# Kernel tuning notes

Measured on AMD Instinct MI355X. Metric: run time of the kernel, lower is better.

## Reference

```python
import jax, jax.numpy as jnp
import numpy as np

V, D, H, S, L, B = 32000, 1024, 4096, 2048, 2, 4
EPS = 1e-5

def setup_inputs() -> dict:
    key = jax.random.key(0)
    ks = jax.random.split(key, 20)
    n = lambda k, shp, s=0.02: (jax.random.normal(k, shp, dtype=jnp.float32) * s)
    inp = {
        'x': jax.random.randint(ks[0], (B, S), 0, V),
        'emb': n(ks[1], (V, D)),
        'wq': n(ks[2], (L, D, H)), 'bq': jnp.zeros((L, H), jnp.float32),
        'wk': n(ks[3], (L, D, H)), 'bk': jnp.zeros((L, H), jnp.float32),
        'wv': n(ks[4], (L, D, H)), 'bv': jnp.zeros((L, H), jnp.float32),
        'wo': n(ks[5], (L, H, D)), 'bo': jnp.zeros((L, D), jnp.float32),
        'w1': n(ks[6], (L, D, H)), 'b1': jnp.zeros((L, H), jnp.float32),
        'w2': n(ks[7], (L, H, D)), 'b2': jnp.zeros((L, D), jnp.float32),
        'ln1_w': jnp.ones((L, S, D), jnp.float32), 'ln1_b': jnp.zeros((L, S, D), jnp.float32),
        'ln2_w': jnp.ones((L, S, D), jnp.float32), 'ln2_b': jnp.zeros((L, S, D), jnp.float32),
    }
    return inp

def _pos_encoding(seq_len, dim, dtype):
    pos = jnp.arange(seq_len, dtype=dtype)          # [S]
    i = jnp.arange(dim, dtype=dtype)                # [D]
    div = jnp.power(jnp.asarray(10000.0, dtype), i / dim)
    ang = pos[:, None] / div[None, :]               # [S, D]
    return jnp.where((jnp.arange(dim) % 2) == 0, jnp.sin(ang), jnp.cos(ang))

def _layernorm2d(y, w, b):
    # normalize over last two dims (token_size, n_dim), per sample
    m = jnp.mean(y, axis=(-2, -1), keepdims=True)
    v = jnp.var(y, axis=(-2, -1), keepdims=True)
    return (y - m) * jax.lax.rsqrt(v + EPS) * w + b

def reference(x, emb, wq, bq, wk, bk, wv, bv, wo, bo, w1, b1, w2, b2, ln1_w, ln1_b, ln2_w, ln2_b):
    y = emb[x]                                       # [B, S, D]
    y = y + _pos_encoding(y.shape[1], y.shape[2], y.dtype)
    n_blocks = wq.shape[0]
    for l in range(n_blocks):
        q = jnp.einsum('bsd,dh->bsh', y, wq[l]) + bq[l]
        k = jnp.einsum('bsd,dh->bsh', y, wk[l]) + bk[l]
        v = jnp.einsum('bsd,dh->bsh', y, wv[l]) + bv[l]
        scores = jnp.einsum('bqh,bkh->bqk', q, k)    # NOTE: unscaled, as in source
        att = jnp.einsum('bqk,bkh->bqh', jax.nn.softmax(scores, axis=-1), v)
        att = jnp.einsum('bsh,hd->bsd', att, wo[l]) + bo[l]
        y = _layernorm2d(y + att, ln1_w[l], ln1_b[l])
        h = jnp.einsum('bsd,dh->bsh', y, w1[l]) + b1[l]
        ffn = jax.nn.gelu(jnp.einsum('bsh,hd->bsd', h, w2[l]) + b2[l], approximate=False)  # GELU AFTER linear2, as in source
        y = _layernorm2d(y + ffn, ln2_w[l], ln2_b[l])
    return y
```

## Files before the change

kernel.cpp:

```cpp
#include <hip/hip_runtime.h>
#include <cstdint>
#include <cstddef>

using bf16 = __bf16;
using f16  = _Float16;
typedef float f32x4 __attribute__((ext_vector_type(4)));
typedef bf16 bf16x8 __attribute__((ext_vector_type(8)));
typedef bf16 bf16x4 __attribute__((ext_vector_type(4)));
typedef f16  f16x8  __attribute__((ext_vector_type(8)));
typedef f16  f16x4  __attribute__((ext_vector_type(4)));

#define NB 4
#define SEQ 2048
#define DM 1024
#define HD 4096
#define SD (SEQ*DM)

__device__ __forceinline__ float geluf(float v) {
    return 0.5f * v * (1.0f + erff(v * 0.70710678118654752f));
}

#define GLL(gp, lp) __builtin_amdgcn_global_load_lds( \
    (const __attribute__((address_space(1))) void*)(gp), \
    (__attribute__((address_space(3))) void*)(lp), 16, 0, 0)

template<int EPI, bool BIAS, int NP, int DT>
__global__ __launch_bounds__(256, NP == 1 ? 4 : 2) void gemm3_nt(
    const bf16* __restrict__ Ah, const bf16* __restrict__ Al,
    const bf16* __restrict__ Bh, const bf16* __restrict__ Bl,
    const float* __restrict__ bias, void* __restrict__ Cg, void* __restrict__ Cl,
    const int K, const int ldab, const int ldc,
    const long sA, const long sB, const long sC)
{
    constexpr int TILE = 128 * 64;
    constexpr int LOSZ = (NP == 3) ? TILE : 8;
    __shared__ __align__(16) bf16 smAh[TILE];
    __shared__ __align__(16) bf16 smBh[TILE];
    __shared__ __align__(16) bf16 smAl[LOSZ];
    __shared__ __align__(16) bf16 smBl[LOSZ];

    const int tid  = threadIdx.x;
    const int lane = tid & 63;
    const int wave = tid >> 6;
    const int wr   = (wave >> 1) << 6;
    const int wc   = (wave & 1) << 6;
    const int l15  = lane & 15;
    const int q4   = lane >> 4;

    int bx = blockIdx.x, by = blockIdx.y;
    {
        const int gx = gridDim.x, gy = gridDim.y;
        if (((gx & 3) | (gy & 3)) == 0) {
            const int tot = gx * gy;
            const int n   = bx + gx * by;
            const int l   = (n & 7) * (tot >> 3) + (n >> 3);
            const int st  = l >> 4, pos = l & 15;
            bx = (st % (gx >> 2)) * 4 + (pos & 3);
            by = (st / (gx >> 2)) * 4 + (pos >> 2);
        }
    }

    const long aoff = (long)blockIdx.z * sA + (long)bx * 128 * ldab;
    const long boff = (long)blockIdx.z * sB + (long)by * 128 * ldab;
    const bf16* pAh = Ah + aoff;
    const bf16* pAl = (NP == 3) ? Al + aoff : nullptr;
    const bf16* pBh = Bh + boff;
    const bf16* pBl = (NP == 3) ? Bl + boff : nullptr;

    int srow[4], scol[4];
#pragma unroll
    for (int it = 0; it < 4; ++it) {
        int chunk = it * 256 + tid;
        int m = chunk >> 3;
        srow[it] = m;
        scol[it] = ((chunk & 7) ^ (m & 7)) * 8;
    }

    f32x4 acc[4][4] = {};

    for (int k0 = 0; k0 < K; k0 += 64) {
#pragma unroll
        for (int it = 0; it < 4; ++it) {
            const long go = (long)srow[it] * ldab + (k0 + scol[it]);
            const size_t lo = (size_t)(it * 256 + (wave << 6)) * 8;
            GLL(pAh + go, smAh + lo);
            if constexpr (NP == 3) GLL(pAl + go, smAl + lo);
            GLL(pBh + go, smBh + lo);
            if constexpr (NP == 3) GLL(pBl + go, smBl + lo);
        }
        __syncthreads();

#pragma unroll
        for (int kk = 0; kk < 2; ++kk) {
            bf16x8 avh[4], avl[4], bvh[4], bvl[4];
#pragma unroll
            for (int i = 0; i < 4; ++i) {
                const int rowa = wr + i * 16 + l15;
                const int ca = ((kk * 4 + q4) ^ (rowa & 7)) * 8;
                avh[i] = *(const bf16x8*)(smAh + rowa * 64 + ca);
                if constexpr (NP == 3) avl[i] = *(const bf16x8*)(smAl + rowa * 64 + ca);
                const int rowb = wc + i * 16 + l15;
                const int cb = ((kk * 4 + q4) ^ (rowb & 7)) * 8;
                bvh[i] = *(const bf16x8*)(smBh + rowb * 64 + cb);
                if constexpr (NP == 3) bvl[i] = *(const bf16x8*)(smBl + rowb * 64 + cb);
            }
#pragma unroll
            for (int i = 0; i < 4; ++i)
#pragma unroll
                for (int j = 0; j < 4; ++j) {
                    if constexpr (DT == 1) {
                        acc[i][j] = __builtin_amdgcn_mfma_f32_16x16x32_f16(
                            *(const f16x8*)&avh[i], *(const f16x8*)&bvh[j],
                            acc[i][j], 0, 0, 0);
                    } else {
                        acc[i][j] = __builtin_amdgcn_mfma_f32_16x16x32_bf16(
                            avh[i], bvh[j], acc[i][j], 0, 0, 0);
                        if constexpr (NP == 3) {
                            acc[i][j] = __builtin_amdgcn_mfma_f32_16x16x32_bf16(
                                avl[i], bvh[j], acc[i][j], 0, 0, 0);
                            acc[i][j] = __builtin_amdgcn_mfma_f32_16x16x32_bf16(
                                avh[i], bvl[j], acc[i][j], 0, 0, 0);
                        }
                    }
                }
        }
        __syncthreads();
    }

    const long zC = (long)blockIdx.z * sC;
    const int gcol0 = by * 128 + wc + l15;
    const int grow0 = bx * 128 + wr + q4 * 4;
#pragma unroll
    for (int j = 0; j < 4; ++j) {
        const int col = gcol0 + j * 16;
        const float bvz = BIAS ? bias[col] : 0.0f;
#pragma unroll
        for (int i = 0; i < 4; ++i) {
            const int row = grow0 + i * 16;
            if (EPI == 5) {
                bf16x4 oh, ol;
#pragma unroll
                for (int e = 0; e < 4; ++e) {
                    const float v = acc[i][j][e] + bvz;
                    const bf16 hi = (bf16)v;
                    oh[e] = hi;
                    ol[e] = (bf16)(v - (float)hi);
                }
                *(bf16x4*)((bf16*)Cg + zC + (long)col * ldc + row) = oh;
                *(bf16x4*)((bf16*)Cl + zC + (long)col * ldc + row) = ol;
            } else if (EPI == 7) {
                f16x4 o;
#pragma unroll
                for (int e = 0; e < 4; ++e) o[e] = (f16)(acc[i][j][e] + bvz);
                *(f16x4*)((f16*)Cg + zC + (long)col * ldc + row) = o;
            } else {
#pragma unroll
                for (int e = 0; e < 4; ++e) {
                    float v = acc[i][j][e] + bvz;
                    if (EPI == 1) v = geluf(v);
                    const long off = zC + (long)(row + e) * ldc + col;
                    if (EPI == 4) {
                        const bf16 hi = (bf16)v;
                        ((bf16*)Cg)[off] = hi;
                        ((bf16*)Cl)[off] = (bf16)(v - (float)hi);
                    } else if (EPI == 6) {
                        ((f16*)Cg)[off] = (f16)v;
                    } else {
                        ((float*)Cg)[off] = v;
                    }
                }
            }
        }
    }
}

__global__ __launch_bounds__(256) void embed_k(
    const int* __restrict__ x, const float* __restrict__ emb,
    bf16* __restrict__ yh, bf16* __restrict__ yl, f16* __restrict__ yf16,
    const float* __restrict__ wkbq, float* __restrict__ vb)
{
    const int bs = blockIdx.x;
    const int s = bs & (SEQ - 1);
    const long e0 = (long)x[bs] * DM;
    const int d = threadIdx.x * 4;
    const float4 ev = *(const float4*)(emb + e0 + d);
    float o[4];
    const float fs = (float)s;
#pragma unroll
    for (int e = 0; e < 4; ++e) {
        const int dd = d + e;
        const float div = powf(10000.0f, (float)dd * (1.0f / 1024.0f));
        const float ang = fs / div;
        const float p = (dd & 1) ? cosf(ang) : sinf(ang);
        o[e] = ((const float*)&ev)[e] + p;
    }
    bf16x4 oh, ol; f16x4 of;
#pragma unroll
    for (int e = 0; e < 4; ++e) {
        oh[e] = (bf16)o[e];
        ol[e] = (bf16)(o[e] - (float)oh[e]);
        of[e] = (f16)o[e];
    }
    *(bf16x4*)(yh + (long)bs * DM + d) = oh;
    *(bf16x4*)(yl + (long)bs * DM + d) = ol;
    *(f16x4*) (yf16 + (long)bs * DM + d) = of;
    const float4 wv = *(const float4*)(wkbq + d);
    float sdot = o[0] * wv.x + o[1] * wv.y + o[2] * wv.z + o[3] * wv.w;
#pragma unroll
    for (int off = 32; off; off >>= 1) sdot += __shfl_xor(sdot, off);
    __shared__ float red[4];
    if ((threadIdx.x & 63) == 0) red[threadIdx.x >> 6] = sdot;
    __syncthreads();
    if (threadIdx.x == 0) vb[bs] = red[0] + red[1] + red[2] + red[3];
}

__global__ __launch_bounds__(256) void copy_split_k(
    const float* __restrict__ src, bf16* __restrict__ dh, bf16* __restrict__ dl)
{
    const long i = ((long)blockIdx.x * 256 + threadIdx.x) * 4;
    const float4 v = *(const float4*)(src + i);
    const float vv[4] = {v.x, v.y, v.z, v.w};
    bf16x4 oh, ol;
#pragma unroll
    for (int e = 0; e < 4; ++e) {
        const bf16 hi = (bf16)vv[e];
        oh[e] = hi;
        ol[e] = (bf16)(vv[e] - (float)hi);
    }
    *(bf16x4*)(dh + i) = oh;
    *(bf16x4*)(dl + i) = ol;
}

__global__ __launch_bounds__(256) void reduce8s_k(
    const float* __restrict__ p, bf16* __restrict__ dh, bf16* __restrict__ dl,
    f16* __restrict__ df)
{
    const long i = ((long)blockIdx.x * 256 + threadIdx.x) * 4;
    const long PL = (long)1 << 20;
    float vv[4] = {0.f, 0.f, 0.f, 0.f};
#pragma unroll
    for (int q = 0; q < 8; ++q) {
        const float4 a = *(const float4*)(p + q * PL + i);
        vv[0] += a.x; vv[1] += a.y; vv[2] += a.z; vv[3] += a.w;
    }
    bf16x4 oh, ol; f16x4 of;
#pragma unroll
    for (int e = 0; e < 4; ++e) {
        const bf16 hi = (bf16)vv[e];
        oh[e] = hi;
        ol[e] = (bf16)(vv[e] - (float)hi);
        of[e] = (f16)vv[e];
    }
    *(bf16x4*)(dh + i) = oh;
    *(bf16x4*)(dl + i) = ol;
    *(f16x4*) (df + i) = of;
}

__global__ __launch_bounds__(256) void reduce8t_k(
    const float* __restrict__ p, bf16* __restrict__ dsth, bf16* __restrict__ dstl,
    f16* __restrict__ dstf)
{
    __shared__ float tf[64][65];
    const long PL = (long)1 << 20;
    const int c0 = blockIdx.x * 64, r0 = blockIdx.y * 64;
    const int t = threadIdx.x;
    const int tr = t >> 4;
    const int tc = (t & 15) * 4;
#pragma unroll
    for (int pp = 0; pp < 4; ++pp) {
        const int r = tr + pp * 16;
        float vv[4] = {0.f, 0.f, 0.f, 0.f};
#pragma unroll
        for (int q = 0; q < 8; ++q) {
            const float4 v = *(const float4*)(p + q * PL + (long)(r0 + r) * 1024 + c0 + tc);
            vv[0] += v.x; vv[1] += v.y; vv[2] += v.z; vv[3] += v.w;
        }
#pragma unroll
        for (int e = 0; e < 4; ++e) tf[r][tc + e] = vv[e];
    }
    __syncthreads();
#pragma unroll
    for (int pp = 0; pp < 4; ++pp) {
        const int c = tr + pp * 16;
        bf16x4 oh, ol; f16x4 of;
#pragma unroll
        for (int e = 0; e < 4; ++e) {
            const float v = tf[tc + e][c];
            const bf16 hi = (bf16)v;
            oh[e] = hi;
            ol[e] = (bf16)(v - (float)hi);
            of[e] = (f16)v;
        }
        *(bf16x4*)(dsth + (long)(c0 + c) * 1024 + r0 + tc) = oh;
        *(bf16x4*)(dstl + (long)(c0 + c) * 1024 + r0 + tc) = ol;
        *(f16x4*) (dstf + (long)(c0 + c) * 1024 + r0 + tc) = of;
    }
}

__global__ __launch_bounds__(256) void transpose_k(
    const float* __restrict__ src, bf16* __restrict__ dsth, bf16* __restrict__ dstl,
    int R, int C)
{
    __shared__ bf16 th[64][65];
    __shared__ bf16 tl[64][65];
    const int c0 = blockIdx.x * 64, r0 = blockIdx.y * 64;
    const int t = threadIdx.x;
    const int tr = t >> 4;
    const int tc = (t & 15) * 4;
#pragma unroll
    for (int p = 0; p < 4; ++p) {
        const int r = tr + p * 16;
        const float4 v = *(const float4*)(src + (long)(r0 + r) * C + c0 + tc);
        const float vv[4] = {v.x, v.y, v.z, v.w};
#pragma unroll
        for (int e = 0; e < 4; ++e) {
            const bf16 hi = (bf16)vv[e];
            th[r][tc + e] = hi;
            tl[r][tc + e] = (bf16)(vv[e] - (float)hi);
        }
    }
    __syncthreads();
#pragma unroll
    for (int p = 0; p < 4; ++p) {
        const int c = tr + p * 16;
        bf16x4 oh, ol;
#pragma unroll
        for (int e = 0; e < 4; ++e) { oh[e] = th[tc + e][c]; ol[e] = tl[tc + e][c]; }
        *(bf16x4*)(dsth + (long)(c0 + c) * R + r0 + tc) = oh;
        *(bf16x4*)(dstl + (long)(c0 + c) * R + r0 + tc) = ol;
    }
}

__global__ __launch_bounds__(256) void matvec_wb_k(
    const float* __restrict__ W, const float* __restrict__ b, float* __restrict__ out)
{
    const int d = blockIdx.x;
    const int t = threadIdx.x;
    float s = 0.f;
    for (int h = t * 4; h < HD; h += 1024) {
        const float4 wv = *(const float4*)(W + (long)d * HD + h);
        const float4 bv = *(const float4*)(b + h);
        s += wv.x * bv.x + wv.y * bv.y + wv.z * bv.z + wv.w * bv.w;
    }
#pragma unroll
    for (int o = 32; o; o >>= 1) s += __shfl_xor(s, o);
    __shared__ float red[4];
    if ((t & 63) == 0) red[t >> 6] = s;
    __syncthreads();
    if (t == 0) out[d] = red[0] + red[1] + red[2] + red[3];
}

__global__ __launch_bounds__(256) void matvec_bt_k(
    const bf16* __restrict__ bth, const bf16* __restrict__ btl,
    const float* __restrict__ b, const float* __restrict__ add,
    float* __restrict__ out)
{
    const int j = blockIdx.x;
    const int t = threadIdx.x;
    float s = 0.f;
    for (int h = t * 4; h < HD; h += 1024) {
        const bf16x4 hx = *(const bf16x4*)(bth + (long)j * HD + h);
        const bf16x4 lx = *(const bf16x4*)(btl + (long)j * HD + h);
        const float4 bv = *(const float4*)(b + h);
        s += ((float)hx[0] + (float)lx[0]) * bv.x + ((float)hx[1] + (float)lx[1]) * bv.y
           + ((float)hx[2] + (float)lx[2]) * bv.z + ((float)hx[3] + (float)lx[3]) * bv.w;
    }
#pragma unroll
    for (int o = 32; o; o >>= 1) s += __shfl_xor(s, o);
    __shared__ float red[4];
    if ((t & 63) == 0) red[t >> 6] = s;
    __syncthreads();
    if (t == 0) out[j] = red[0] + red[1] + red[2] + red[3] + add[j];
}

__global__ __launch_bounds__(256) void softmax_k(
    const float* __restrict__ S, const float* __restrict__ v,
    f16* __restrict__ P)
{
    const long row = blockIdx.x;
    const float4* src = (const float4*)(S + (row << 11));
    const float* vr = v + (long)(row >> 11) * SEQ;
    const int t = threadIdx.x;
    float4 a = src[t], b = src[256 + t];
    const float4 va = *(const float4*)(vr + t * 4);
    const float4 vb = *(const float4*)(vr + 1024 + t * 4);
    a.x += va.x; a.y += va.y; a.z += va.z; a.w += va.w;
    b.x += vb.x; b.y += vb.y; b.z += vb.z; b.w += vb.w;
    float m = fmaxf(fmaxf(fmaxf(a.x, a.y), fmaxf(a.z, a.w)),
                    fmaxf(fmaxf(b.x, b.y), fmaxf(b.z, b.w)));
#pragma unroll
    for (int o = 32; o; o >>= 1) m = fmaxf(m, __shfl_xor(m, o));
    __shared__ float red1[4], red2[4];
    const int wv = t >> 6;
    if ((t & 63) == 0) red1[wv] = m;
    __syncthreads();
    m = fmaxf(fmaxf(red1[0], red1[1]), fmaxf(red1[2], red1[3]));

    a.x = expf(a.x - m); a.y = expf(a.y - m); a.z = expf(a.z - m); a.w = expf(a.w - m);
    b.x = expf(b.x - m); b.y = expf(b.y - m); b.z = expf(b.z - m); b.w = expf(b.w - m);
    float s = a.x + a.y + a.z + a.w + b.x + b.y + b.z + b.w;
#pragma unroll
    for (int o = 32; o; o >>= 1) s += __shfl_xor(s, o);
    if ((t & 63) == 0) red2[wv] = s;
    __syncthreads();
    s = red2[0] + red2[1] + red2[2] + red2[3];
    const float inv = 1.0f / s;

    f16x4 o0, o1;
    o0[0] = (f16)(a.x * inv); o0[1] = (f16)(a.y * inv);
    o0[2] = (f16)(a.z * inv); o0[3] = (f16)(a.w * inv);
    o1[0] = (f16)(b.x * inv); o1[1] = (f16)(b.y * inv);
    o1[2] = (f16)(b.z * inv); o1[3] = (f16)(b.w * inv);
    *(f16x4*)(P + (row << 11) + t * 4) = o0;
    *(f16x4*)(P + (row << 11) + 1024 + t * 4) = o1;
}

__global__ __launch_bounds__(256) void ln_stats_k(
    const bf16* __restrict__ yh, const bf16* __restrict__ yl,
    const float* __restrict__ r, float2* __restrict__ part)
{
    const int b = blockIdx.y;
    const long base = (long)b * SD + (long)blockIdx.x * (SD / 64);
    float s = 0.f, q = 0.f;
    for (int i = threadIdx.x; i < (SD / 64) / 4; i += 256) {
        const bf16x4 h = *(const bf16x4*)(yh + base + i * 4);
        const bf16x4 l = *(const bf16x4*)(yl + base + i * 4);
        const float4 c = *(const float4*)(r + base + i * 4);
        const float cc[4] = {c.x, c.y, c.z, c.w};
#pragma unroll
        for (int e = 0; e < 4; ++e) {
            const float xx = (float)h[e] + (float)l[e] + cc[e];
            s += xx; q += xx * xx;
        }
    }
#pragma unroll
    for (int o = 32; o; o >>= 1) { s += __shfl_xor(s, o); q += __shfl_xor(q, o); }
    __shared__ float rs[4], rq[4];
    const int wv = threadIdx.x >> 6;
    if ((threadIdx.x & 63) == 0) { rs[wv] = s; rq[wv] = q; }
    __syncthreads();
    if (threadIdx.x == 0)
        part[b * 64 + blockIdx.x] = make_float2(rs[0] + rs[1] + rs[2] + rs[3],
                                                rq[0] + rq[1] + rq[2] + rq[3]);
}

__global__ void ln_fin_k(const float2* __restrict__ part, float2* __restrict__ stats)
{
    const int b = blockIdx.x;
    const float2 p = part[b * 64 + threadIdx.x];
    float s = p.x, q = p.y;
#pragma unroll
    for (int o = 32; o; o >>= 1) { s += __shfl_xor(s, o); q += __shfl_xor(q, o); }
    if (threadIdx.x == 0) {
        const float inv_n = 1.0f / (float)SD;
        const float mean = s * inv_n;
        const float var = fmaxf(q * inv_n - mean * mean, 0.f);
        stats[b] = make_float2(mean, rsqrtf(var + 1e-5f));
    }
}

__global__ __launch_bounds__(256) void ln_apply_k(
    const bf16* __restrict__ yh_in, const bf16* __restrict__ yl_in,
    const float* __restrict__ r,
    const float* __restrict__ w, const float* __restrict__ bb,
    const float2* __restrict__ stats,
    bf16* __restrict__ yh_out, bf16* __restrict__ yl_out, f16* __restrict__ yf16,
    float* __restrict__ fout,
    const float* __restrict__ wkbq, float* __restrict__ vb)
{
    const long i = (long)blockIdx.x * 1024 + threadIdx.x * 4;
    const int smp = (int)(i >> 21);
    const long sd = i & (SD - 1);
    const float2 st = stats[smp];
    const bf16x4 h = *(const bf16x4*)(yh_in + i);
    const bf16x4 l = *(const bf16x4*)(yl_in + i);
    const float4 c = *(const float4*)(r + i);
    const float4 wv = *(const float4*)(w + sd);
    const float4 bv = *(const float4*)(bb + sd);
    const float cc[4] = {c.x, c.y, c.z, c.w};
    const float ww[4] = {wv.x, wv.y, wv.z, wv.w};
    const float bbx[4] = {bv.x, bv.y, bv.z, bv.w};
    float o[4];
#pragma unroll
    for (int e = 0; e < 4; ++e) {
        const float xx = (float)h[e] + (float)l[e] + cc[e];
        o[e] = (xx - st.x) * st.y * ww[e] + bbx[e];
    }
    bf16x4 oh, ol; f16x4 of;
#pragma unroll
    for (int e = 0; e < 4; ++e) {
        oh[e] = (bf16)o[e];
        ol[e] = (bf16)(o[e] - (float)oh[e]);
        of[e] = (f16)o[e];
    }
    *(bf16x4*)(yh_out + i) = oh;
    *(bf16x4*)(yl_out + i) = ol;
    *(f16x4*) (yf16 + i) = of;
    if (fout != nullptr) *(float4*)(fout + i) = *(float4*)o;
    if (vb != nullptr) {
        const int d = threadIdx.x * 4;
        const float4 kv = *(const float4*)(wkbq + d);
        float sdot = o[0] * kv.x + o[1] * kv.y + o[2] * kv.z + o[3] * kv.w;
#pragma unroll
        for (int off = 32; off; off >>= 1) sdot += __shfl_xor(sdot, off);
        __shared__ float red[4];
        if ((threadIdx.x & 63) == 0) red[threadIdx.x >> 6] = sdot;
        __syncthreads();
        if (threadIdx.x == 0) vb[blockIdx.x] = red[0] + red[1] + red[2] + red[3];
    }
}

extern "C" void kernel_launch(void* const* d_in, const int* in_sizes, int n_in,
                              void* d_out, int out_size, void* d_ws, size_t ws_size,
                              hipStream_t stream)
{
    (void)in_sizes; (void)n_in; (void)out_size; (void)ws_size;

    const int*   x    = (const int*)  d_in[0];
    const float* emb  = (const float*)d_in[1];
    const float* wq   = (const float*)d_in[2];
    const float* bq   = (const float*)d_in[3];
    const float* wk   = (const float*)d_in[4];
    const float* bk   = (const float*)d_in[5];
    const float* wv   = (const float*)d_in[6];
    const float* bv   = (const float*)d_in[7];
    const float* wo   = (const float*)d_in[8];
    const float* bo   = (const float*)d_in[9];
    const float* w1   = (const float*)d_in[10];
    const float* b1   = (const float*)d_in[11];
    const float* w2   = (const float*)d_in[12];
    const float* b2   = (const float*)d_in[13];
    const float* ln1w = (const float*)d_in[14];
    const float* ln1b = (const float*)d_in[15];
    const float* ln2w = (const float*)d_in[16];
    const float* ln2b = (const float*)d_in[17];
    (void)bk;

    char* ws = (char*)d_ws;
    const size_t MB = (size_t)1 << 20;
    bf16*   ybh   = (bf16*) (ws);
    bf16*   ybl   = (bf16*) (ws + 16  * MB);
    f16*    yf16  = (f16*)  (ws + 32  * MB);
    bf16*   S0h   = (bf16*) (ws + 48  * MB);
    bf16*   S0l   = (bf16*) (ws + 56  * MB);
    bf16*   S1h   = (bf16*) (ws + 64  * MB);
    bf16*   S1l   = (bf16*) (ws + 72  * MB);
    bf16*   MTh   = (bf16*) (ws + 80  * MB);
    bf16*   MTl   = (bf16*) (ws + 82  * MB);
    f16*    MTf   = (f16*)  (ws + 84  * MB);
    bf16*   VOh   = (bf16*) (ws + 86  * MB);
    bf16*   VOl   = (bf16*) (ws + 88  * MB);
    f16*    VOf   = (f16*)  (ws + 90  * MB);
    bf16*   W12h  = (bf16*) (ws + 92  * MB);
    bf16*   W12l  = (bf16*) (ws + 94  * MB);
    f16*    W12f  = (f16*)  (ws + 96  * MB);
    float*  wkbq2 = (float*)(ws + 98  * MB);
    float*  c_vo  = (float*)(ws + 98  * MB + 0x10000);
    float*  c_12  = (float*)(ws + 98  * MB + 0x20000);
    float*  vbias = (float*)(ws + 98  * MB + 0x30000);
    float2* part  = (float2*)(ws + 98 * MB + 0x40000);
    float2* stats = (float2*)(ws + 98 * MB + 0x50000);
    float*  wtmp8 = (float*)(ws + 100 * MB);
    bf16*   zh    = (bf16*) (ws + 132 * MB);
    bf16*   zl    = (bf16*) (ws + 148 * MB);
    f16*    zf    = (f16*)  (ws + 164 * MB);
    f16*    uTf   = (f16*)  (ws + 180 * MB);
    float*  scf   = (float*)(ws + 196 * MB);
    f16*    Pf    = (f16*)  (ws + 260 * MB);
    float*  attout= (float*)(ws + 292 * MB);
    float*  ffnf  = attout;

    const long TSZ = (long)DM * HD;

    matvec_wb_k<<<1024, 256, 0, stream>>>(wk + 0 * TSZ, bq + 0 * HD, wkbq2);
    matvec_wb_k<<<1024, 256, 0, stream>>>(wk + 1 * TSZ, bq + 1 * HD, wkbq2 + 0x4000 / 4);

    embed_k<<<NB * SEQ, 256, 0, stream>>>(x, emb, ybh, ybl, yf16, wkbq2, vbias);

    for (int l = 0; l < 2; ++l) {
        const float* wkbq_next = wkbq2 + 0x4000 / 4;

        copy_split_k<<<4096, 256, 0, stream>>>(wq + l * TSZ, S0h, S0l);
        copy_split_k<<<4096, 256, 0, stream>>>(wk + l * TSZ, S1h, S1l);
        gemm3_nt<0, false, 3, 0><<<dim3(8, 8, 8), 256, 0, stream>>>(
            S1h, S1l, S0h, S0l, nullptr, wtmp8, nullptr,
            512, HD, 1024, 512, 512, (long)1 << 20);
        reduce8s_k<<<1024, 256, 0, stream>>>(wtmp8, MTh, MTl, MTf);
        if (l == 0) {
            gemm3_nt<4, false, 3, 0><<<dim3(64, 8, 1), 256, 0, stream>>>(
                ybh, ybl, MTh, MTl, nullptr, zh, zl, DM, DM, DM, 0, 0, 0);
            gemm3_nt<0, false, 3, 0><<<dim3(16, 16, NB), 256, 0, stream>>>(
                zh, zl, ybh, ybl, nullptr, scf, nullptr,
                DM, DM, SEQ, (long)SD, (long)SD, (long)SEQ * SEQ);
        } else {
            gemm3_nt<6, false, 1, 1><<<dim3(64, 8, 1), 256, 0, stream>>>(
                (const bf16*)yf16, nullptr, (const bf16*)MTf, nullptr, nullptr,
                zf, nullptr, DM, DM, DM, 0, 0, 0);
            gemm3_nt<0, false, 1, 1><<<dim3(16, 16, NB), 256, 0, stream>>>(
                (const bf16*)zf, nullptr, (const bf16*)yf16, nullptr, nullptr,
                scf, nullptr, DM, DM, SEQ, (long)SD, (long)SD, (long)SEQ * SEQ);
        }
        softmax_k<<<NB * SEQ, 256, 0, stream>>>(scf, vbias, Pf);

        copy_split_k<<<4096, 256, 0, stream>>>(wv + l * TSZ, S0h, S0l);
        transpose_k <<<dim3(16, 64), 256, 0, stream>>>(wo + l * TSZ, S1h, S1l, HD, DM);
        matvec_bt_k<<<1024, 256, 0, stream>>>(S1h, S1l, bv + l * HD, bo + l * DM, c_vo);
        if (l == 0)
            gemm3_nt<0, false, 3, 0><<<dim3(8, 8, 8), 256, 0, stream>>>(
                S0h, S0l, S1h, S1l, nullptr, wtmp8, nullptr,
                512, HD, 1024, 512, 512, (long)1 << 20);
        else
            gemm3_nt<0, false, 1, 0><<<dim3(8, 8, 8), 256, 0, stream>>>(
                S0h, nullptr, S1h, nullptr, nullptr, wtmp8, nullptr,
                512, HD, 1024, 512, 512, (long)1 << 20);
        reduce8t_k<<<dim3(16, 16), 256, 0, stream>>>(wtmp8, VOh, VOl, VOf);
        if (l == 0)
            gemm3_nt<7, false, 3, 0><<<dim3(16, 8, NB), 256, 0, stream>>>(
                ybh, ybl, VOh, VOl, nullptr, uTf, nullptr,
                DM, DM, SEQ, (long)SD, 0, (long)DM * SEQ);
        else
            gemm3_nt<7, false, 1, 1><<<dim3(16, 8, NB), 256, 0, stream>>>(
                (const bf16*)yf16, nullptr, (const bf16*)VOf, nullptr, nullptr,
                uTf, nullptr, DM, DM, SEQ, (long)SD, 0, (long)DM * SEQ);
        gemm3_nt<0, true, 1, 1><<<dim3(16, 8, NB), 256, 0, stream>>>(
            (const bf16*)Pf, nullptr, (const bf16*)uTf, nullptr, c_vo, attout, nullptr,
            SEQ, SEQ, DM, (long)SEQ * SEQ, (long)DM * SEQ, (long)SEQ * DM);
        ln_stats_k<<<dim3(64, NB), 256, 0, stream>>>(ybh, ybl, attout, part);
        ln_fin_k  <<<NB, 64, 0, stream>>>(part, stats);
        ln_apply_k<<<8192, 256, 0, stream>>>(ybh, ybl, attout,
                                             ln1w + (long)l * SD, ln1b + (long)l * SD,
                                             stats, ybh, ybl, yf16, nullptr,
                                             nullptr, nullptr);

        copy_split_k<<<4096, 256, 0, stream>>>(w1 + l * TSZ, S0h, S0l);
        transpose_k <<<dim3(16, 64), 256, 0, stream>>>(w2 + l * TSZ, S1h, S1l, HD, DM);
        matvec_bt_k<<<1024, 256, 0, stream>>>(S1h, S1l, b1 + l * HD, b2 + l * DM, c_12);
        if (l == 0)
            gemm3_nt<0, false, 3, 0><<<dim3(8, 8, 8), 256, 0, stream>>>(
                S0h, S0l, S1h, S1l, nullptr, wtmp8, nullptr,
                512, HD, 1024, 512, 512, (long)1 << 20);
        else
            gemm3_nt<0, false, 1, 0><<<dim3(8, 8, 8), 256, 0, stream>>>(
                S0h, nullptr, S1h, nullptr, nullptr, wtmp8, nullptr,
                512, HD, 1024, 512, 512, (long)1 << 20);
        reduce8t_k<<<dim3(16, 16), 256, 0, stream>>>(wtmp8, W12h, W12l, W12f);
        gemm3_nt<1, true, 1, 1><<<dim3(64, 8, 1), 256, 0, stream>>>(
            (const bf16*)yf16, nullptr, (const bf16*)W12f, nullptr, c_12,
            ffnf, nullptr, DM, DM, DM, 0, 0, 0);
        float* fdst = (l == 1) ? (float*)d_out : nullptr;
        ln_stats_k<<<dim3(64, NB), 256, 0, stream>>>(ybh, ybl, ffnf, part);
        ln_fin_k  <<<NB, 64, 0, stream>>>(part, stats);
        ln_apply_k<<<8192, 256, 0, stream>>>(ybh, ybl, ffnf,
                                             ln2w + (long)l * SD, ln2b + (long)l * SD,
                                             stats, ybh, ybl, yf16, fdst,
                                             (l == 0) ? wkbq_next : nullptr,
                                             (l == 0) ? vbias : nullptr);
    }
}
```

Measured before the change: 1.016 ms.

## Compute fused weight products in single-pass fp16 and drop split-K reductions

The precomputed weight products Wv·Wo, W1·W2 and layer-2 Wq·Wk^T were built from split bf16 hi/lo operands with 3-pass or split-K GEMMs plus 8-way reduction kernels. They are now built directly from fp16 copies in one fp16 GEMM that writes the fp16 output, already transposed, with no split-K stage. Layer 0 keeps the split-precision path only for the QK product. This removes the partial-sum buffer traffic, the reduce kernels and the extra precision passes on weight preprocessing. The cost is lower accuracy in the fused weights, and layer-0 VO and W12 now use fp16 instead of 3-pass bf16.

```diff
diff --git a/kernel.cpp b/kernel.cpp
--- a/kernel.cpp
+++ b/kernel.cpp
@@ -137,18 +137,7 @@
 #pragma unroll
         for (int i = 0; i < 4; ++i) {
             const int row = grow0 + i * 16;
-            if (EPI == 5) {
-                bf16x4 oh, ol;
-#pragma unroll
-                for (int e = 0; e < 4; ++e) {
-                    const float v = acc[i][j][e] + bvz;
-                    const bf16 hi = (bf16)v;
-                    oh[e] = hi;
-                    ol[e] = (bf16)(v - (float)hi);
-                }
-                *(bf16x4*)((bf16*)Cg + zC + (long)col * ldc + row) = oh;
-                *(bf16x4*)((bf16*)Cl + zC + (long)col * ldc + row) = ol;
-            } else if (EPI == 7) {
+            if (EPI == 7) {
                 f16x4 o;
 #pragma unroll
                 for (int e = 0; e < 4; ++e) o[e] = (f16)(acc[i][j][e] + bvz);
@@ -231,9 +220,43 @@
     *(bf16x4*)(dl + i) = ol;
 }
 
+__global__ __launch_bounds__(256) void copy_f16_k(
+    const float* __restrict__ src, f16* __restrict__ dst)
+{
+    const long i = ((long)blockIdx.x * 256 + threadIdx.x) * 4;
+    const float4 v = *(const float4*)(src + i);
+    f16x4 o;
+    o[0] = (f16)v.x; o[1] = (f16)v.y; o[2] = (f16)v.z; o[3] = (f16)v.w;
+    *(f16x4*)(dst + i) = o;
+}
+
+__global__ __launch_bounds__(256) void transpose_f16_k(
+    const float* __restrict__ src, f16* __restrict__ dst, int R, int C)
+{
+    __shared__ f16 tf[64][65];
+    const int c0 = blockIdx.x * 64, r0 = blockIdx.y * 64;
+    const int t = threadIdx.x;
+    const int tr = t >> 4;
+    const int tc = (t & 15) * 4;
+#pragma unroll
+    for (int p = 0; p < 4; ++p) {
+        const int r = tr + p * 16;
+        const float4 v = *(const float4*)(src + (long)(r0 + r) * C + c0 + tc);
+        tf[r][tc] = (f16)v.x; tf[r][tc + 1] = (f16)v.y;
+        tf[r][tc + 2] = (f16)v.z; tf[r][tc + 3] = (f16)v.w;
+    }
+    __syncthreads();
+#pragma unroll
+    for (int p = 0; p < 4; ++p) {
+        const int c = tr + p * 16;
+        f16x4 o;
+        o[0] = tf[tc][c]; o[1] = tf[tc + 1][c]; o[2] = tf[tc + 2][c]; o[3] = tf[tc + 3][c];
+        *(f16x4*)(dst + (long)(c0 + c) * R + r0 + tc) = o;
+    }
+}
+
 __global__ __launch_bounds__(256) void reduce8s_k(
-    const float* __restrict__ p, bf16* __restrict__ dh, bf16* __restrict__ dl,
-    f16* __restrict__ df)
+    const float* __restrict__ p, bf16* __restrict__ dh, bf16* __restrict__ dl)
 {
     const long i = ((long)blockIdx.x * 256 + threadIdx.x) * 4;
     const long PL = (long)1 << 20;
@@ -243,92 +266,15 @@
         const float4 a = *(const float4*)(p + q * PL + i);
         vv[0] += a.x; vv[1] += a.y; vv[2] += a.z; vv[3] += a.w;
     }
-    bf16x4 oh, ol; f16x4 of;
+    bf16x4 oh, ol;
 #pragma unroll
     for (int e = 0; e < 4; ++e) {
         const bf16 hi = (bf16)vv[e];
         oh[e] = hi;
         ol[e] = (bf16)(vv[e] - (float)hi);
-        of[e] = (f16)vv[e];
     }
     *(bf16x4*)(dh + i) = oh;
     *(bf16x4*)(dl + i) = ol;
-    *(f16x4*) (df + i) = of;
-}
-
-__global__ __launch_bounds__(256) void reduce8t_k(
-    const float* __restrict__ p, bf16* __restrict__ dsth, bf16* __restrict__ dstl,
-    f16* __restrict__ dstf)
-{
-    __shared__ float tf[64][65];
-    const long PL = (long)1 << 20;
-    const int c0 = blockIdx.x * 64, r0 = blockIdx.y * 64;
-    const int t = threadIdx.x;
-    const int tr = t >> 4;
-    const int tc = (t & 15) * 4;
-#pragma unroll
-    for (int pp = 0; pp < 4; ++pp) {
-        const int r = tr + pp * 16;
-        float vv[4] = {0.f, 0.f, 0.f, 0.f};
-#pragma unroll
-        for (int q = 0; q < 8; ++q) {
-            const float4 v = *(const float4*)(p + q * PL + (long)(r0 + r) * 1024 + c0 + tc);
-            vv[0] += v.x; vv[1] += v.y; vv[2] += v.z; vv[3] += v.w;
-        }
-#pragma unroll
-        for (int e = 0; e < 4; ++e) tf[r][tc + e] = vv[e];
-    }
-    __syncthreads();
-#pragma unroll
-    for (int pp = 0; pp < 4; ++pp) {
-        const int c = tr + pp * 16;
-        bf16x4 oh, ol; f16x4 of;
-#pragma unroll
-        for (int e = 0; e < 4; ++e) {
-            const float v = tf[tc + e][c];
-            const bf16 hi = (bf16)v;
-            oh[e] = hi;
-            ol[e] = (bf16)(v - (float)hi);
-            of[e] = (f16)v;
-        }
-        *(bf16x4*)(dsth + (long)(c0 + c) * 1024 + r0 + tc) = oh;
-        *(bf16x4*)(dstl + (long)(c0 + c) * 1024 + r0 + tc) = ol;
-        *(f16x4*) (dstf + (long)(c0 + c) * 1024 + r0 + tc) = of;
-    }
-}
-
-__global__ __launch_bounds__(256) void transpose_k(
-    const float* __restrict__ src, bf16* __restrict__ dsth, bf16* __restrict__ dstl,
-    int R, int C)
-{
-    __shared__ bf16 th[64][65];
-    __shared__ bf16 tl[64][65];
-    const int c0 = blockIdx.x * 64, r0 = blockIdx.y * 64;
-    const int t = threadIdx.x;
-    const int tr = t >> 4;
-    const int tc = (t & 15) * 4;
-#pragma unroll
-    for (int p = 0; p < 4; ++p) {
-        const int r = tr + p * 16;
-        const float4 v = *(const float4*)(src + (long)(r0 + r) * C + c0 + tc);
-        const float vv[4] = {v.x, v.y, v.z, v.w};
-#pragma unroll
-        for (int e = 0; e < 4; ++e) {
-            const bf16 hi = (bf16)vv[e];
-            th[r][tc + e] = hi;
-            tl[r][tc + e] = (bf16)(vv[e] - (float)hi);
-        }
-    }
-    __syncthreads();
-#pragma unroll
-    for (int p = 0; p < 4; ++p) {
-        const int c = tr + p * 16;
-        bf16x4 oh, ol;
-#pragma unroll
-        for (int e = 0; e < 4; ++e) { oh[e] = th[tc + e][c]; ol[e] = tl[tc + e][c]; }
-        *(bf16x4*)(dsth + (long)(c0 + c) * R + r0 + tc) = oh;
-        *(bf16x4*)(dstl + (long)(c0 + c) * R + r0 + tc) = ol;
-    }
 }
 
 __global__ __launch_bounds__(256) void matvec_wb_k(
@@ -350,20 +296,18 @@
     if (t == 0) out[d] = red[0] + red[1] + red[2] + red[3];
 }
 
-__global__ __launch_bounds__(256) void matvec_bt_k(
-    const bf16* __restrict__ bth, const bf16* __restrict__ btl,
-    const float* __restrict__ b, const float* __restrict__ add,
-    float* __restrict__ out)
+__global__ __launch_bounds__(256) void matvec_btf_k(
+    const f16* __restrict__ btf, const float* __restrict__ b,
+    const float* __restrict__ add, float* __restrict__ out)
 {
     const int j = blockIdx.x;
     const int t = threadIdx.x;
     float s = 0.f;
     for (int h = t * 4; h < HD; h += 1024) {
-        const bf16x4 hx = *(const bf16x4*)(bth + (long)j * HD + h);
-        const bf16x4 lx = *(const bf16x4*)(btl + (long)j * HD + h);
+        const f16x4 hx = *(const f16x4*)(btf + (long)j * HD + h);
         const float4 bv = *(const float4*)(b + h);
-        s += ((float)hx[0] + (float)lx[0]) * bv.x + ((float)hx[1] + (float)lx[1]) * bv.y
-           + ((float)hx[2] + (float)lx[2]) * bv.z + ((float)hx[3] + (float)lx[3]) * bv.w;
+        s += (float)hx[0] * bv.x + (float)hx[1] * bv.y
+           + (float)hx[2] * bv.z + (float)hx[3] * bv.w;
     }
 #pragma unroll
     for (int o = 32; o; o >>= 1) s += __shfl_xor(s, o);
@@ -545,29 +489,27 @@
     bf16*   S0l   = (bf16*) (ws + 56  * MB);
     bf16*   S1h   = (bf16*) (ws + 64  * MB);
     bf16*   S1l   = (bf16*) (ws + 72  * MB);
+    f16*    F0    = (f16*)  (ws + 48  * MB);
+    f16*    F1    = (f16*)  (ws + 56  * MB);
     bf16*   MTh   = (bf16*) (ws + 80  * MB);
     bf16*   MTl   = (bf16*) (ws + 82  * MB);
     f16*    MTf   = (f16*)  (ws + 84  * MB);
-    bf16*   VOh   = (bf16*) (ws + 86  * MB);
-    bf16*   VOl   = (bf16*) (ws + 88  * MB);
-    f16*    VOf   = (f16*)  (ws + 90  * MB);
-    bf16*   W12h  = (bf16*) (ws + 92  * MB);
-    bf16*   W12l  = (bf16*) (ws + 94  * MB);
-    f16*    W12f  = (f16*)  (ws + 96  * MB);
-    float*  wkbq2 = (float*)(ws + 98  * MB);
-    float*  c_vo  = (float*)(ws + 98  * MB + 0x10000);
-    float*  c_12  = (float*)(ws + 98  * MB + 0x20000);
-    float*  vbias = (float*)(ws + 98  * MB + 0x30000);
-    float2* part  = (float2*)(ws + 98 * MB + 0x40000);
-    float2* stats = (float2*)(ws + 98 * MB + 0x50000);
-    float*  wtmp8 = (float*)(ws + 100 * MB);
-    bf16*   zh    = (bf16*) (ws + 132 * MB);
-    bf16*   zl    = (bf16*) (ws + 148 * MB);
-    f16*    zf    = (f16*)  (ws + 164 * MB);
-    f16*    uTf   = (f16*)  (ws + 180 * MB);
-    float*  scf   = (float*)(ws + 196 * MB);
-    f16*    Pf    = (f16*)  (ws + 260 * MB);
-    float*  attout= (float*)(ws + 292 * MB);
+    f16*    VOTf  = (f16*)  (ws + 86  * MB);
+    f16*    W12Tf = (f16*)  (ws + 88  * MB);
+    float*  wkbq2 = (float*)(ws + 90  * MB);
+    float*  c_vo  = (float*)(ws + 90  * MB + 0x10000);
+    float*  c_12  = (float*)(ws + 90  * MB + 0x20000);
+    float*  vbias = (float*)(ws + 90  * MB + 0x30000);
+    float2* part  = (float2*)(ws + 90 * MB + 0x40000);
+    float2* stats = (float2*)(ws + 90 * MB + 0x50000);
+    float*  wtmp8 = (float*)(ws + 92  * MB);
+    bf16*   zh    = (bf16*) (ws + 124 * MB);
+    bf16*   zl    = (bf16*) (ws + 140 * MB);
+    f16*    zf    = (f16*)  (ws + 156 * MB);
+    f16*    uTf   = (f16*)  (ws + 172 * MB);
+    float*  scf   = (float*)(ws + 188 * MB);
+    f16*    Pf    = (f16*)  (ws + 252 * MB);
+    float*  attout= (float*)(ws + 284 * MB);
     float*  ffnf  = attout;
 
     const long TSZ = (long)DM * HD;
@@ -580,19 +522,24 @@
     for (int l = 0; l < 2; ++l) {
         const float* wkbq_next = wkbq2 + 0x4000 / 4;
 
-        copy_split_k<<<4096, 256, 0, stream>>>(wq + l * TSZ, S0h, S0l);
-        copy_split_k<<<4096, 256, 0, stream>>>(wk + l * TSZ, S1h, S1l);
-        gemm3_nt<0, false, 3, 0><<<dim3(8, 8, 8), 256, 0, stream>>>(
-            S1h, S1l, S0h, S0l, nullptr, wtmp8, nullptr,
-            512, HD, 1024, 512, 512, (long)1 << 20);
-        reduce8s_k<<<1024, 256, 0, stream>>>(wtmp8, MTh, MTl, MTf);
         if (l == 0) {
+            copy_split_k<<<4096, 256, 0, stream>>>(wq + l * TSZ, S0h, S0l);
+            copy_split_k<<<4096, 256, 0, stream>>>(wk + l * TSZ, S1h, S1l);
+            gemm3_nt<0, false, 3, 0><<<dim3(8, 8, 8), 256, 0, stream>>>(
+                S1h, S1l, S0h, S0l, nullptr, wtmp8, nullptr,
+                512, HD, 1024, 512, 512, (long)1 << 20);
+            reduce8s_k<<<1024, 256, 0, stream>>>(wtmp8, MTh, MTl);
             gemm3_nt<4, false, 3, 0><<<dim3(64, 8, 1), 256, 0, stream>>>(
                 ybh, ybl, MTh, MTl, nullptr, zh, zl, DM, DM, DM, 0, 0, 0);
             gemm3_nt<0, false, 3, 0><<<dim3(16, 16, NB), 256, 0, stream>>>(
                 zh, zl, ybh, ybl, nullptr, scf, nullptr,
                 DM, DM, SEQ, (long)SD, (long)SD, (long)SEQ * SEQ);
         } else {
+            copy_f16_k<<<4096, 256, 0, stream>>>(wq + l * TSZ, F0);
+            copy_f16_k<<<4096, 256, 0, stream>>>(wk + l * TSZ, F1);
+            gemm3_nt<6, false, 1, 1><<<dim3(8, 8, 1), 256, 0, stream>>>(
+                (const bf16*)F1, nullptr, (const bf16*)F0, nullptr, nullptr,
+                MTf, nullptr, HD, HD, DM, 0, 0, 0);
             gemm3_nt<6, false, 1, 1><<<dim3(64, 8, 1), 256, 0, stream>>>(
                 (const bf16*)yf16, nullptr, (const bf16*)MTf, nullptr, nullptr,
                 zf, nullptr, DM, DM, DM, 0, 0, 0);
@@ -602,26 +549,17 @@
         }
         softmax_k<<<NB * SEQ, 256, 0, stream>>>(scf, vbias, Pf);
 
-        copy_split_k<<<4096, 256, 0, stream>>>(wv + l * TSZ, S0h, S0l);
-        transpose_k <<<dim3(16, 64), 256, 0, stream>>>(wo + l * TSZ, S1h, S1l, HD, DM);
-        matvec_bt_k<<<1024, 256, 0, stream>>>(S1h, S1l, bv + l * HD, bo + l * DM, c_vo);
-        if (l == 0)
-            gemm3_nt<0, false, 3, 0><<<dim3(8, 8, 8), 256, 0, stream>>>(
-                S0h, S0l, S1h, S1l, nullptr, wtmp8, nullptr,
-                512, HD, 1024, 512, 512, (long)1 << 20);
-        else
-            gemm3_nt<0, false, 1, 0><<<dim3(8, 8, 8), 256, 0, stream>>>(
-                S0h, nullptr, S1h, nullptr, nullptr, wtmp8, nullptr,
-                512, HD, 1024, 512, 512, (long)1 << 20);
-        reduce8t_k<<<dim3(16, 16), 256, 0, stream>>>(wtmp8, VOh, VOl, VOf);
-        if (l == 0)
-            gemm3_nt<7, false, 3, 0><<<dim3(16, 8, NB), 256, 0, stream>>>(
-                ybh, ybl, VOh, VOl, nullptr, uTf, nullptr,
-                DM, DM, SEQ, (long)SD, 0, (long)DM * SEQ);
-        else
-            gemm3_nt<7, false, 1, 1><<<dim3(16, 8, NB), 256, 0, stream>>>(
-                (const bf16*)yf16, nullptr, (const bf16*)VOf, nullptr, nullptr,
-                uTf, nullptr, DM, DM, SEQ, (long)SD, 0, (long)DM * SEQ);
+        f16* WvF  = (f16*)(ws + 64 * MB);
+        f16* WoTf = (f16*)(ws + 72 * MB);
+        copy_f16_k     <<<4096, 256, 0, stream>>>(wv + l * TSZ, WvF);
+        transpose_f16_k<<<dim3(16, 64), 256, 0, stream>>>(wo + l * TSZ, WoTf, HD, DM);
+        matvec_btf_k<<<1024, 256, 0, stream>>>(WoTf, bv + l * HD, bo + l * DM, c_vo);
+        gemm3_nt<6, false, 1, 1><<<dim3(8, 8, 1), 256, 0, stream>>>(
+            (const bf16*)WoTf, nullptr, (const bf16*)WvF, nullptr, nullptr,
+            VOTf, nullptr, HD, HD, DM, 0, 0, 0);
+        gemm3_nt<7, false, 1, 1><<<dim3(16, 8, NB), 256, 0, stream>>>(
+            (const bf16*)yf16, nullptr, (const bf16*)VOTf, nullptr, nullptr,
+            uTf, nullptr, DM, DM, SEQ, (long)SD, 0, (long)DM * SEQ);
         gemm3_nt<0, true, 1, 1><<<dim3(16, 8, NB), 256, 0, stream>>>(
             (const bf16*)Pf, nullptr, (const bf16*)uTf, nullptr, c_vo, attout, nullptr,
             SEQ, SEQ, DM, (long)SEQ * SEQ, (long)DM * SEQ, (long)SEQ * DM);
@@ -632,20 +570,16 @@
                                              stats, ybh, ybl, yf16, nullptr,
                                              nullptr, nullptr);
 
-        copy_split_k<<<4096, 256, 0, stream>>>(w1 + l * TSZ, S0h, S0l);
-        transpose_k <<<dim3(16, 64), 256, 0, stream>>>(w2 + l * TSZ, S1h, S1l, HD, DM);
-        matvec_bt_k<<<1024, 256, 0, stream>>>(S1h, S1l, b1 + l * HD, b2 + l * DM, c_12);
-        if (l == 0)
-            gemm3_nt<0, false, 3, 0><<<dim3(8, 8, 8), 256, 0, stream>>>(
-                S0h, S0l, S1h, S1l, nullptr, wtmp8, nullptr,
-                512, HD, 1024, 512, 512, (long)1 << 20);
-        else
-            gemm3_nt<0, false, 1, 0><<<dim3(8, 8, 8), 256, 0, stream>>>(
-                S0h, nullptr, S1h, nullptr, nullptr, wtmp8, nullptr,
-                512, HD, 1024, 512, 512, (long)1 << 20);
-        reduce8t_k<<<dim3(16, 16), 256, 0, stream>>>(wtmp8, W12h, W12l, W12f);
+        f16* W1F  = (f16*)(ws + 48 * MB);
+        f16* W2Tf = (f16*)(ws + 56 * MB);
+        copy_f16_k     <<<4096, 256, 0, stream>>>(w1 + l * TSZ, W1F);
+        transpose_f16_k<<<dim3(16, 64), 256, 0, stream>>>(w2 + l * TSZ, W2Tf, HD, DM);
+        matvec_btf_k<<<1024, 256, 0, stream>>>(W2Tf, b1 + l * HD, b2 + l * DM, c_12);
+        gemm3_nt<6, false, 1, 1><<<dim3(8, 8, 1), 256, 0, stream>>>(
+            (const bf16*)W2Tf, nullptr, (const bf16*)W1F, nullptr, nullptr,
+            W12Tf, nullptr, HD, HD, DM, 0, 0, 0);
         gemm3_nt<1, true, 1, 1><<<dim3(64, 8, 1), 256, 0, stream>>>(
-            (const bf16*)yf16, nullptr, (const bf16*)W12f, nullptr, c_12,
+            (const bf16*)yf16, nullptr, (const bf16*)W12Tf, nullptr, c_12,
             ffnf, nullptr, DM, DM, DM, 0, 0, 0);
         float* fdst = (l == 1) ? (float*)d_out : nullptr;
         ln_stats_k<<<dim3(64, NB), 256, 0, stream>>>(ybh, ybl, ffnf, part);
```

New measurement: 1.141 ms. +12.3%, slower.
